# Kernel optimization log

Measured on AMD Instinct MI355X. Metric: run time of the kernel, lower is better.

The kernel has to match this reference:

```python
import jax, jax.numpy as jnp
import numpy as np


def setup_inputs() -> dict:
    key = jax.random.key(0)
    k1, k2 = jax.random.split(key)
    B, A, K = 4096, 10000, 128
    x = jax.random.normal(k1, (B, A), dtype=jnp.float32)
    possible_moves = jax.random.randint(k2, (B, K), 0, A, dtype=jnp.int64)
    return {"x": x, "possible_moves": possible_moves}


def reference(x, possible_moves):
    # Build legal-move mask: mask[i, possible_moves[i]] = 1.0 (one fused scatter,
    # no Python loop over batch).
    B = x.shape[0]
    rows = jnp.arange(B)[:, None]  # [B, 1] broadcasts against [B, K] indices
    mask = jnp.zeros_like(x).at[rows, possible_moves].set(1.0)
    filtered = x * mask
    # Original: filtered_actions[filtered_actions == 0] = -inf
    return jnp.where(filtered == 0.0, -jnp.inf, filtered)
```

## Files before the change

kernel.cpp:

```cpp
#include <hip/hip_runtime.h>


#define A_DIM 10000
#define K_DIM 128
#define NEG_FILL (-1.0e38f)

__global__ __launch_bounds__(256) void FilterLegalMoves_kernel(
    const float* __restrict__ x,
    const int* __restrict__ moves,
    float* __restrict__ out)
{
    const int row = blockIdx.x;
    const long long base = (long long)row * A_DIM;

    float4* out4 = reinterpret_cast<float4*>(out + base);
    const int n4 = A_DIM / 4;
    const float4 fill4 = make_float4(NEG_FILL, NEG_FILL, NEG_FILL, NEG_FILL);
    for (int j = threadIdx.x; j < n4; j += blockDim.x) {
        out4[j] = fill4;
    }

    __syncthreads();

    if (threadIdx.x < K_DIM) {
        const int idx = moves[(long long)row * K_DIM + threadIdx.x];
        const float v = x[base + idx];
        out[base + idx] = (v == 0.0f) ? NEG_FILL : v;
    }
}

extern "C" void kernel_launch(void* const* d_in, const int* in_sizes, int n_in,
                              void* d_out, int out_size, void* d_ws, size_t ws_size,
                              hipStream_t stream) {
    const float* x    = (const float*)d_in[0];
    const int* moves  = (const int*)d_in[1];
    float* out        = (float*)d_out;

    const int B = in_sizes[0] / A_DIM;
    FilterLegalMoves_kernel<<<B, 256, 0, stream>>>(x, moves, out);
}
```

Before: 272.4 us.

## Build per-row shared-memory bitmask and write output in one float4 pass

Each block first builds a bitmask of the row's legal moves in shared memory with atomicOr. It then writes the whole row with float4 stores in a single pass, loading a float4 of x only when its nibble of the mask is nonzero. This replaces the fill pass followed by 128 scattered read-modify-writes with one coalesced write stream plus a few sparse reads. The cost is an extra barrier and shared-memory atomics. Many x float4 groups are still loaded, about 5% of the row, since each touched group is read in full.

```diff
diff --git a/kernel.cpp b/kernel.cpp
--- a/kernel.cpp
+++ b/kernel.cpp
@@ -1,8 +1,9 @@
 #include <hip/hip_runtime.h>
 
 
-#define A_DIM 10000
-#define K_DIM 128
+#define A_DIM  10000
+#define K_DIM  128
+#define NWORDS 313
 #define NEG_FILL (-1.0e38f)
 
 __global__ __launch_bounds__(256) void FilterLegalMoves_kernel(
@@ -10,31 +11,44 @@
     const int* __restrict__ moves,
     float* __restrict__ out)
 {
+    __shared__ unsigned int bits[NWORDS];
+    const int tid = threadIdx.x;
     const int row = blockIdx.x;
     const long long base = (long long)row * A_DIM;
 
-    float4* out4 = reinterpret_cast<float4*>(out + base);
-    const int n4 = A_DIM / 4;
-    const float4 fill4 = make_float4(NEG_FILL, NEG_FILL, NEG_FILL, NEG_FILL);
-    for (int j = threadIdx.x; j < n4; j += blockDim.x) {
-        out4[j] = fill4;
-    }
-
+    for (int w = tid; w < NWORDS; w += 256) bits[w] = 0u;
     __syncthreads();
 
-    if (threadIdx.x < K_DIM) {
-        const int idx = moves[(long long)row * K_DIM + threadIdx.x];
-        const float v = x[base + idx];
-        out[base + idx] = (v == 0.0f) ? NEG_FILL : v;
+    if (tid < K_DIM) {
+        const int idx = moves[(long long)row * K_DIM + tid];
+        atomicOr(&bits[idx >> 5], 1u << (idx & 31));
+    }
+    __syncthreads();
+
+    const float4* __restrict__ x4 = reinterpret_cast<const float4*>(x + base);
+    float4*       __restrict__ o4 = reinterpret_cast<float4*>(out + base);
+    const int n4 = A_DIM / 4;
+    for (int g = tid; g < n4; g += 256) {
+        const int j = g * 4;
+        const unsigned nib = (bits[j >> 5] >> (j & 31)) & 0xFu;
+        float4 r = make_float4(NEG_FILL, NEG_FILL, NEG_FILL, NEG_FILL);
+        if (nib) {
+            const float4 v = x4[g];
+            if ((nib & 1u) && v.x != 0.0f) r.x = v.x;
+            if ((nib & 2u) && v.y != 0.0f) r.y = v.y;
+            if ((nib & 4u) && v.z != 0.0f) r.z = v.z;
+            if ((nib & 8u) && v.w != 0.0f) r.w = v.w;
+        }
+        o4[g] = r;
     }
 }
 
 extern "C" void kernel_launch(void* const* d_in, const int* in_sizes, int n_in,
                               void* d_out, int out_size, void* d_ws, size_t ws_size,
                               hipStream_t stream) {
-    const float* x    = (const float*)d_in[0];
-    const int* moves  = (const int*)d_in[1];
-    float* out        = (float*)d_out;
+    const float* x   = (const float*)d_in[0];
+    const int* moves = (const int*)d_in[1];
+    float* out       = (float*)d_out;
 
     const int B = in_sizes[0] / A_DIM;
     FilterLegalMoves_kernel<<<B, 256, 0, stream>>>(x, moves, out);
```

Result: faster. 265.3 us (-2.6%).

## Split fill and scatter into separate flat-grid kernels

Applied to the files above, without the earlier changes.

Replaces the per-row kernel, which filled a row and then scattered after a block barrier, with two launches. The first kernel writes the sentinel fill over the whole output as a flat float4 grid, one element per thread. The second scatters the legal-move values, one thread per (row, move). This drops the per-row strided loop and the barrier and gives the fill a fully parallel grid, in exchange for an extra launch and a second pass over the scattered locations. The sentinel value is -1e38 rather than -inf, and the output where x is zero is unchanged from before.

```diff
diff --git a/kernel.cpp b/kernel.cpp
--- a/kernel.cpp
+++ b/kernel.cpp
@@ -1,41 +1,46 @@
 #include <hip/hip_runtime.h>
 
 
-#define A_DIM 10000
-#define K_DIM 128
+#define A_DIM  10000
+#define K_DIM  128
 #define NEG_FILL (-1.0e38f)
 
-__global__ __launch_bounds__(256) void FilterLegalMoves_kernel(
+__global__ __launch_bounds__(256) void fill_sentinel_kernel(
+    float4* __restrict__ out4, int n4)
+{
+    const int i = blockIdx.x * 256 + threadIdx.x;
+    if (i < n4) {
+        out4[i] = make_float4(NEG_FILL, NEG_FILL, NEG_FILL, NEG_FILL);
+    }
+}
+
+__global__ __launch_bounds__(256) void scatter_legal_kernel(
     const float* __restrict__ x,
     const int* __restrict__ moves,
-    float* __restrict__ out)
+    float* __restrict__ out, int total)
 {
-    const int row = blockIdx.x;
+    const int flat = blockIdx.x * 256 + threadIdx.x;
+    if (flat >= total) return;
+    const int row = flat >> 7;
     const long long base = (long long)row * A_DIM;
-
-    float4* out4 = reinterpret_cast<float4*>(out + base);
-    const int n4 = A_DIM / 4;
-    const float4 fill4 = make_float4(NEG_FILL, NEG_FILL, NEG_FILL, NEG_FILL);
-    for (int j = threadIdx.x; j < n4; j += blockDim.x) {
-        out4[j] = fill4;
-    }
-
-    __syncthreads();
-
-    if (threadIdx.x < K_DIM) {
-        const int idx = moves[(long long)row * K_DIM + threadIdx.x];
-        const float v = x[base + idx];
-        out[base + idx] = (v == 0.0f) ? NEG_FILL : v;
-    }
+    const int idx = moves[flat];
+    const float v = x[base + idx];
+    out[base + idx] = (v == 0.0f) ? NEG_FILL : v;
 }
 
 extern "C" void kernel_launch(void* const* d_in, const int* in_sizes, int n_in,
                               void* d_out, int out_size, void* d_ws, size_t ws_size,
                               hipStream_t stream) {
-    const float* x    = (const float*)d_in[0];
-    const int* moves  = (const int*)d_in[1];
-    float* out        = (float*)d_out;
+    const float* x   = (const float*)d_in[0];
+    const int* moves = (const int*)d_in[1];
+    float* out       = (float*)d_out;
 
-    const int B = in_sizes[0] / A_DIM;
-    FilterLegalMoves_kernel<<<B, 256, 0, stream>>>(x, moves, out);
+    const int n4 = out_size / 4;
+    const int fill_blocks = (n4 + 255) / 256;
+    fill_sentinel_kernel<<<fill_blocks, 256, 0, stream>>>(
+        reinterpret_cast<float4*>(out), n4);
+
+    const int total = in_sizes[1];
+    const int sc_blocks = (total + 255) / 256;
+    scatter_legal_kernel<<<sc_blocks, 256, 0, stream>>>(x, moves, out, total);
 }
```

Result: slower. 278.5 us (+2.2%).
